# Kernel tuning notes

Measured on AMD Instinct MI355X. Metric: run time of the kernel, lower is better.

The kernel has to match this reference:

```python
import jax, jax.numpy as jnp
import numpy as np
import math

B, S, K, H, NH = 4, 1024, 512, 1024, 16
HD = H // NH  # 64


def _split_heads(x):
    # [B, L, H] -> [B, NH, L, HD]
    b, l, _ = x.shape
    return x.reshape(b, l, NH, HD).transpose(0, 2, 1, 3)


def setup_inputs() -> dict:
    key = jax.random.key(0)
    ks = jax.random.split(key, 16)
    scale = 1.0 / math.sqrt(H)
    d = {
        'hidden_states': jax.random.normal(ks[0], (B, S, H), jnp.float32),
        'encoder_hidden_states': jax.random.normal(ks[1], (B, K, H), jnp.float32),
        'attention_mask': jnp.zeros((B, 1, 1, S), jnp.float32),
        'encoder_attention_mask': jnp.zeros((B, 1, 1, K), jnp.float32),
    }
    names = ['q', 'k', 'v', 'kq', 'kk', 'kv']
    for i, n in enumerate(names):
        d[f'W{n}'] = jax.random.normal(ks[2 + i], (H, H), jnp.float32) * scale
        d[f'b{n}'] = jnp.zeros((H,), jnp.float32)
    return d


def reference(hidden_states, encoder_hidden_states, attention_mask, encoder_attention_mask,
              Wq, bq, Wk, bk, Wv, bv, Wkq, bkq, Wkk, bkk, Wkv, bkv):
    inv = 1.0 / math.sqrt(HD)
    # self branch
    q = _split_heads(hidden_states @ Wq + bq)            # [B,NH,S,HD]
    k = _split_heads(hidden_states @ Wk + bk)
    v = _split_heads(hidden_states @ Wv + bv)
    scores = jnp.einsum('bhsd,bhtd->bhst', q, k) * inv + attention_mask
    probs = jax.nn.softmax(scores, axis=-1)              # [B,NH,S,S]
    ctx = jnp.einsum('bhst,bhtd->bhsd', probs, v)
    # knowledge branch
    kq = _split_heads(hidden_states @ Wkq + bkq)          # [B,NH,S,HD]
    kk = _split_heads(encoder_hidden_states @ Wkk + bkk)  # [B,NH,K,HD]
    kv = _split_heads(encoder_hidden_states @ Wkv + bkv)
    kscores = jnp.einsum('bhsd,bhtd->bhst', kq, kk) * inv + encoder_attention_mask
    kprobs = jax.nn.softmax(kscores, axis=-1)            # [B,NH,S,K]
    kctx = jnp.einsum('bhst,bhtd->bhsd', kprobs, kv)
    # merge heads and average branches
    out = (ctx + kctx) * 0.5                             # [B,NH,S,HD]
    out = out.transpose(0, 2, 1, 3).reshape(B, S, H)
    return out
```

## Files before the change

kernel.cpp:

```cpp
#include <hip/hip_runtime.h>

#define BATCH 4
#define SEQ   1024
#define KENC  512
#define HDIM  1024
#define NHEAD 16
#define HD    64
#define LOG2E 1.44269504088896340736f

typedef __attribute__((ext_vector_type(8))) short bf16x8;
typedef __attribute__((ext_vector_type(4))) float f32x4;
typedef __attribute__((ext_vector_type(16))) float f32x16;
typedef __attribute__((ext_vector_type(4))) float f4v;
typedef __attribute__((ext_vector_type(4))) short s4v;

__device__ __forceinline__ short f2bf(float f) {
  unsigned u = __float_as_uint(f);
  u += 0x7fffu + ((u >> 16) & 1u);
  return (short)(u >> 16);
}

__device__ __forceinline__ void gload_lds16(const void* g, void* l) {
  __builtin_amdgcn_global_load_lds(
      (const __attribute__((address_space(1))) void*)g,
      (__attribute__((address_space(3))) void*)l, 16, 0, 0);
}

#define MF(A, B, C) __builtin_amdgcn_mfma_f32_16x16x32_bf16((A), (B), (C), 0, 0, 0)

__global__ __launch_bounds__(256) void cast2(const float* __restrict__ sa,
                                             short* __restrict__ da, int n4a,
                                             const float* __restrict__ sb,
                                             short* __restrict__ db, int n4b) {
  int i = blockIdx.x * 256 + threadIdx.x;
  const float* s;
  short* d;
  int j;
  if (i < n4a) { s = sa; d = da; j = i; }
  else { j = i - n4a; if (j >= n4b) return; s = sb; d = db; }
  f4v v = ((const f4v*)s)[j];
  s4v o;
#pragma unroll
  for (int k = 0; k < 4; ++k) o[k] = f2bf(v[k]);
  ((s4v*)d)[j] = o;
}

struct WtArgs { const float* W[6]; };

__global__ __launch_bounds__(256) void wt_cast(WtArgs a, short* __restrict__ wt) {
  int j = blockIdx.z;
  const float* W = a.W[j];
  short* dst = wt + (size_t)j * (HDIM * HDIM);
  int cb = blockIdx.x * 32, rb = blockIdx.y * 32;
  __shared__ float t[32][33];
  int tx = threadIdx.x & 31, ty = threadIdx.x >> 5;
#pragma unroll
  for (int rr = 0; rr < 4; ++rr)
    t[ty + rr * 8][tx] = W[(size_t)(rb + ty + rr * 8) * HDIM + cb + tx];
  __syncthreads();
#pragma unroll
  for (int rr = 0; rr < 4; ++rr)
    dst[(size_t)(cb + ty + rr * 8) * HDIM + rb + tx] = f2bf(t[tx][ty + rr * 8]);
}

struct ProjArgs {
  const short* X[6];
  const short* Wt[6];
  const float* bias[6];
  short* out[6];
  int tshift[6];
  int mode[6];
  float scale[6];
};

__global__ __launch_bounds__(256) void proj_gemm(ProjArgs a) {
  int lid = blockIdx.x;
  int t = (lid & 7) * 160 + (lid >> 3);
  int job, bx, by;
  if (t < 1024) { job = t >> 8; int r = t & 255; bx = r & 7; by = r >> 3; }
  else { int u = t - 1024; job = 4 + (u >> 7); int r = u & 127; bx = r & 7; by = r >> 3; }

  const short* X = a.X[job];
  const short* W = a.Wt[job];

  __shared__ __align__(16) char Lds[65536];

  int tid = threadIdx.x, lane = tid & 63, wave = tid >> 6;
  int wr = wave >> 1, wc = wave & 1;
  int l15 = lane & 15, g4 = lane >> 4;

  f32x4 acc[4][4];
#pragma unroll
  for (int m = 0; m < 4; ++m)
#pragma unroll
    for (int n = 0; n < 4; ++n)
#pragma unroll
      for (int r = 0; r < 4; ++r) acc[m][n][r] = 0.0f;

  int arow = by * 128, brow = bx * 128;
  const int crow = lane >> 2;
  const int sgrp = (lane & 3) ^ ((lane >> 2) & 3) ^ (lane >> 4);
  const int rsw = (lane & 3) ^ (l15 >> 2);

  const char* Xb = (const char*)X;
  const char* Wb = (const char*)W;
  const size_t sac0 = ((size_t)(arow + 32 * wave + crow) * HDIM + sgrp * 8) * 2;
  const size_t sac1 = sac0 + (size_t)16 * HDIM * 2;
  const size_t sbc0 = ((size_t)(brow + 32 * wave + crow) * HDIM + sgrp * 8) * 2;
  const size_t sbc1 = sbc0 + (size_t)16 * HDIM * 2;
  const int ldA0 = wave * 2048, ldA1 = ldA0 + 1024;
  const int ldB0 = 8192 + ldA0, ldB1 = ldB0 + 1024;

  const int aoff = wr * 4096 + l15 * 64 + ((g4 ^ rsw) << 4);
  const int boff = 8192 + wc * 4096 + l15 * 64 + ((g4 ^ rsw) << 4);

#define STG_A(SBO, SKT)                                                  \
  do {                                                                   \
    gload_lds16(Xb + sac0 + (size_t)(SKT) * 64, Lds + (SBO) + ldA0);     \
    gload_lds16(Xb + sac1 + (size_t)(SKT) * 64, Lds + (SBO) + ldA1);     \
  } while (0)
#define STG_B(SBO, SKT)                                                  \
  do {                                                                   \
    gload_lds16(Wb + sbc0 + (size_t)(SKT) * 64, Lds + (SBO) + ldB0);     \
    gload_lds16(Wb + sbc1 + (size_t)(SKT) * 64, Lds + (SBO) + ldB1);     \
  } while (0)

  STG_A(0, 0);     STG_B(0, 0);
  STG_A(16384, 1); STG_B(16384, 1);
  STG_A(32768, 2); STG_B(32768, 2);
  asm volatile("s_waitcnt vmcnt(8)" ::: "memory");
  __builtin_amdgcn_s_barrier();
  asm volatile("" ::: "memory");

#define STEP(BO, DO_STG, SBO, SKT, VMW, ENDBAR)                               \
  do {                                                                        \
                   \
    bf16x8 a0 = *(const bf16x8*)(Lds + (BO) + 0 * 1024 + aoff);               \
    bf16x8 a1 = *(const bf16x8*)(Lds + (BO) + 1 * 1024 + aoff);               \
    bf16x8 b0 = *(const bf16x8*)(Lds + (BO) + 0 * 1024 + boff);               \
    bf16x8 b1 = *(const bf16x8*)(Lds + (BO) + 1 * 1024 + boff);               \
    bf16x8 b2 = *(const bf16x8*)(Lds + (BO) + 2 * 1024 + boff);               \
    bf16x8 b3 = *(const bf16x8*)(Lds + (BO) + 3 * 1024 + boff);               \
    if (DO_STG) STG_A(SBO, SKT);                                              \
    __builtin_amdgcn_sched_barrier(0);                                        \
    __builtin_amdgcn_s_barrier();                                             \
    asm volatile("s_waitcnt lgkmcnt(0)" ::: "memory");                        \
    __builtin_amdgcn_sched_barrier(0);                                        \
    __builtin_amdgcn_s_setprio(1);                                            \
    acc[0][0] = MF(a0, b0, acc[0][0]);                                        \
    acc[0][1] = MF(a0, b1, acc[0][1]);                                        \
    acc[0][2] = MF(a0, b2, acc[0][2]);                                        \
    acc[0][3] = MF(a0, b3, acc[0][3]);                                        \
    acc[1][0] = MF(a1, b0, acc[1][0]);                                        \
    acc[1][1] = MF(a1, b1, acc[1][1]);                                        \
    acc[1][2] = MF(a1, b2, acc[1][2]);                                        \
    acc[1][3] = MF(a1, b3, acc[1][3]);                                        \
    __builtin_amdgcn_s_setprio(0);                                            \
    __builtin_amdgcn_sched_barrier(0);                                        \
    __builtin_amdgcn_s_barrier();                                             \
                    \
    bf16x8 a2 = *(const bf16x8*)(Lds + (BO) + 2 * 1024 + aoff);               \
    bf16x8 a3 = *(const bf16x8*)(Lds + (BO) + 3 * 1024 + aoff);               \
    if (DO_STG) STG_B(SBO, SKT);                                              \
    __builtin_amdgcn_sched_barrier(0);                                        \
    __builtin_amdgcn_s_barrier();                                             \
    asm volatile("s_waitcnt lgkmcnt(0)" ::: "memory");                        \
    __builtin_amdgcn_sched_barrier(0);                                        \
    __builtin_amdgcn_s_setprio(1);                                            \
    acc[2][0] = MF(a2, b0, acc[2][0]);                                        \
    acc[2][1] = MF(a2, b1, acc[2][1]);                                        \
    acc[2][2] = MF(a2, b2, acc[2][2]);                                        \
    acc[2][3] = MF(a2, b3, acc[2][3]);                                        \
    acc[3][0] = MF(a3, b0, acc[3][0]);                                        \
    acc[3][1] = MF(a3, b1, acc[3][1]);                                        \
    acc[3][2] = MF(a3, b2, acc[3][2]);                                        \
    acc[3][3] = MF(a3, b3, acc[3][3]);                                        \
    __builtin_amdgcn_s_setprio(0);                                            \
    asm volatile(VMW ::: "memory");                                           \
    __builtin_amdgcn_sched_barrier(0);                                        \
    if (ENDBAR) {                                                             \
      __builtin_amdgcn_s_barrier();                                           \
      asm volatile("" ::: "memory");                                          \
    }                                                                         \
  } while (0)

#pragma unroll 1
  for (int tt = 0; tt < 29; ++tt) {
    int bo = (tt & 3) << 14;
    int sbo = ((tt + 3) & 3) << 14;
    STEP(bo, 1, sbo, tt + 3, "s_waitcnt vmcnt(8)", 1);
  }
  STEP((29 & 3) << 14, 0, 0, 0, "s_waitcnt vmcnt(4)", 1);
  STEP((30 & 3) << 14, 0, 0, 0, "s_waitcnt vmcnt(0)", 1);
  STEP((31 & 3) << 14, 0, 0, 0, "s_nop 0", 0);

#undef STEP
#undef STG_A
#undef STG_B

  const float* bias = a.bias[job];
  short* out = a.out[job];
  int tshift = a.tshift[job], tmask = (1 << tshift) - 1, mode = a.mode[job];
  float scl = a.scale[job];
#pragma unroll
  for (int m = 0; m < 4; ++m) {
    int rowb = arow + wr * 64 + m * 16 + (g4 << 2);
#pragma unroll
    for (int n = 0; n < 4; ++n) {
      int col = brow + wc * 64 + n * 16 + l15;
      float bv = bias[col];
      int head = col >> 6, d = col & 63;
#pragma unroll
      for (int r = 0; r < 4; ++r) {
        int row = rowb + r;
        int bb = row >> tshift, tk = row & tmask;
        float val = (acc[m][n][r] + bv) * scl;
        size_t idx;
        if (mode == 0)
          idx = ((((size_t)bb * NHEAD + head) << tshift) + tk) * 64 + d;
        else
          idx = ((((size_t)bb * NHEAD + head) * 64 + d) << tshift) + tk;
        out[idx] = f2bf(val);
      }
    }
  }
}

__global__ __launch_bounds__(256, 3) void attn32(
    const short* __restrict__ qall, const short* __restrict__ kall,
    const short* __restrict__ vTall, const short* __restrict__ kqall,
    const short* __restrict__ kkall, const short* __restrict__ kvTall,
    const float* __restrict__ amask, const float* __restrict__ emask,
    float* __restrict__ out) {
  __shared__ char KT[2][8192];
  __shared__ char VT[2][8192];
  __shared__ float red[4][32];

  int lid = blockIdx.x;
  int id = (lid & 7) * 64 + (lid >> 3);
  int bh = id >> 3, qb = id & 7;
  int b = bh >> 4, h = bh & 15;
  int lane = threadIdx.x & 63, wave = threadIdx.x >> 6;
  int l31 = lane & 31, hi = lane >> 5, x7 = l31 & 7;
  int qrow0 = qb * 128 + wave * 32;

  bf16x8 qcur[4];
  {
    const short* qp = qall + ((size_t)bh * SEQ + qrow0 + l31) * 64;
#pragma unroll
    for (int i = 0; i < 4; ++i)
      qcur[i] = *(const bf16x8*)(qp + i * 16 + hi * 8);
  }

  const char* kb0 = (const char*)(kall + (size_t)bh * SEQ * 64);
  const char* vb0 = (const char*)(vTall + (size_t)bh * 64 * SEQ);
  const char* kb1 = (const char*)(kkall + (size_t)bh * KENC * 64);
  const char* vb1 = (const char*)(kvTall + (size_t)bh * 64 * KENC);
  const float* mpc = amask + (size_t)b * SEQ;

  auto STAGE = [&](int pb, const char* kb, const char* vb, size_t vrowb, int kt) {
    int t0 = threadIdx.x;
#pragma unroll
    for (int c = 0; c < 2; ++c) {
      int idx = c * 256 + t0;
      int row = idx >> 3, phys = idx & 7;
      int lg = phys ^ (row & 7);
      gload_lds16(kb + ((size_t)(kt * 64 + row)) * 128 + lg * 16,
                  KT[pb] + idx * 16);
      gload_lds16(vb + (size_t)row * vrowb + (size_t)kt * 128 + lg * 16,
                  VT[pb] + idx * 16);
    }
  };

  STAGE(0, kb0, vb0, SEQ * 2, 0);

  f32x16 ctx0, ctx1, c10, c11;
#pragma unroll
  for (int r = 0; r < 16; ++r) { ctx0[r] = 0.f; ctx1[r] = 0.f; c10[r] = 0.f; c11[r] = 0.f; }
  float mr = -1e30f, lr = 0.f;

#pragma unroll 1
  for (int t = 0; t < 24; ++t) {
    int p = t & 1;
    __syncthreads();
    if (t < 23) {
      int tn = t + 1;
      if (tn >= 16) STAGE(p ^ 1, kb1, vb1, KENC * 2, tn - 16);
      else          STAGE(p ^ 1, kb0, vb0, SEQ * 2, tn);
    }
    if (t == 16) {
      if (!hi) red[wave][l31] = lr;
      asm volatile("s_waitcnt lgkmcnt(0)" ::: "memory");
#pragma unroll
      for (int r2 = 0; r2 < 4; ++r2) {
        f4v lv = *(const f4v*)(&red[wave][r2 * 8 + 4 * hi]);
#pragma unroll
        for (int j2 = 0; j2 < 4; ++j2) {
          float li = __builtin_amdgcn_rcpf(lv[j2]);
          int r = r2 * 4 + j2;
          c10[r] = ctx0[r] * li;  ctx0[r] = 0.f;
          c11[r] = ctx1[r] * li;  ctx1[r] = 0.f;
        }
      }
      mr = -1e30f; lr = 0.f;
      const short* kqp = kqall + ((size_t)bh * SEQ + qrow0 + l31) * 64;
#pragma unroll
      for (int i = 0; i < 4; ++i)
        qcur[i] = *(const bf16x8*)(kqp + i * 16 + hi * 8);
      mpc = emask + (size_t)b * KENC;
    }
    int kt = (t >= 16) ? t - 16 : t;
    const char* Kp = KT[p];
    const char* Vp = VT[p];

    f32x16 s0, s1;
#pragma unroll
    for (int r = 0; r < 16; ++r) { s0[r] = 0.f; s1[r] = 0.f; }
    __builtin_amdgcn_s_setprio(1);
#pragma unroll
    for (int i = 0; i < 4; ++i) {
      bf16x8 kf = *(const bf16x8*)(Kp + (l31)*128 + (((2 * i + hi) ^ x7) << 4));
      s0 = __builtin_amdgcn_mfma_f32_32x32x16_bf16(kf, qcur[i], s0, 0, 0, 0);
    }
#pragma unroll
    for (int i = 0; i < 4; ++i) {
      bf16x8 kf = *(const bf16x8*)(Kp + (32 + l31) * 128 + (((2 * i + hi) ^ x7) << 4));
      s1 = __builtin_amdgcn_mfma_f32_32x32x16_bf16(kf, qcur[i], s1, 0, 0, 0);
    }
    __builtin_amdgcn_s_setprio(0);

    const float* mp = mpc + kt * 64;
#pragma unroll
    for (int r2 = 0; r2 < 4; ++r2) {
      f4v ma = *(const f4v*)(mp + r2 * 8 + 4 * hi);
      f4v mb = *(const f4v*)(mp + 32 + r2 * 8 + 4 * hi);
#pragma unroll
      for (int j2 = 0; j2 < 4; ++j2) {
        s0[r2 * 4 + j2] = fmaf(ma[j2], LOG2E, s0[r2 * 4 + j2]);
        s1[r2 * 4 + j2] = fmaf(mb[j2], LOG2E, s1[r2 * 4 + j2]);
      }
    }

    float mx = s0[0];
#pragma unroll
    for (int r = 1; r < 16; ++r) mx = fmaxf(mx, s0[r]);
#pragma unroll
    for (int r = 0; r < 16; ++r) mx = fmaxf(mx, s1[r]);
    mx = fmaxf(mx, __int_as_float(__shfl_xor(__float_as_int(mx), 32)));

    if (!__all(mx <= mr + 12.f)) {
      float mn = fmaxf(mr, mx);
      float scl = __builtin_amdgcn_exp2f(mr - mn);
      mr = mn; lr *= scl;
      if (!hi) red[wave][l31] = scl;
      asm volatile("s_waitcnt lgkmcnt(0)" ::: "memory");
#pragma unroll
      for (int r2 = 0; r2 < 4; ++r2) {
        f4v sv = *(const f4v*)(&red[wave][r2 * 8 + 4 * hi]);
#pragma unroll
        for (int j2 = 0; j2 < 4; ++j2) {
          ctx0[r2 * 4 + j2] *= sv[j2];
          ctx1[r2 * 4 + j2] *= sv[j2];
        }
      }
    }

    float rs = 0.f;
#pragma unroll
    for (int r = 0; r < 16; ++r) { s0[r] = __builtin_amdgcn_exp2f(s0[r] - mr); rs += s0[r]; }
#pragma unroll
    for (int r = 0; r < 16; ++r) { s1[r] = __builtin_amdgcn_exp2f(s1[r] - mr); rs += s1[r]; }
    rs += __int_as_float(__shfl_xor(__float_as_int(rs), 32));
    lr += rs;

#pragma unroll
    for (int s = 0; s < 2; ++s) {
      const f32x16& sv = s ? s1 : s0;
      unsigned W[8];
#pragma unroll
      for (int r2 = 0; r2 < 4; ++r2) {
        asm("v_cvt_pk_bf16_f32 %0, %1, %2"
            : "=v"(W[r2 * 2]) : "v"(sv[r2 * 4 + 0]), "v"(sv[r2 * 4 + 1]));
        asm("v_cvt_pk_bf16_f32 %0, %1, %2"
            : "=v"(W[r2 * 2 + 1]) : "v"(sv[r2 * 4 + 2]), "v"(sv[r2 * 4 + 3]));
      }
#pragma unroll
      for (int jr = 0; jr < 2; ++jr) {
        unsigned sendA = hi ? W[(2 * jr) * 2]     : W[(2 * jr + 1) * 2];
        unsigned sendB = hi ? W[(2 * jr) * 2 + 1] : W[(2 * jr + 1) * 2 + 1];
        unsigned rA = (unsigned)__shfl_xor((int)sendA, 32);
        unsigned rB = (unsigned)__shfl_xor((int)sendB, 32);
        union { unsigned u[4]; bf16x8 v; } pa;
        if (!hi) { pa.u[0] = W[2 * jr * 2]; pa.u[1] = W[2 * jr * 2 + 1];
                   pa.u[2] = rA;            pa.u[3] = rB; }
        else     { pa.u[0] = rA;            pa.u[1] = rB;
                   pa.u[2] = W[(2 * jr + 1) * 2]; pa.u[3] = W[(2 * jr + 1) * 2 + 1]; }
        int j = s * 2 + jr;
        __builtin_amdgcn_s_setprio(1);
        bf16x8 vf0 = *(const bf16x8*)(Vp + (l31)*128 + (((2 * j + hi) ^ x7) << 4));
        ctx0 = __builtin_amdgcn_mfma_f32_32x32x16_bf16(pa.v, vf0, ctx0, 0, 0, 0);
        bf16x8 vf1 = *(const bf16x8*)(Vp + (32 + l31) * 128 + (((2 * j + hi) ^ x7) << 4));
        ctx1 = __builtin_amdgcn_mfma_f32_32x32x16_bf16(pa.v, vf1, ctx1, 0, 0, 0);
        __builtin_amdgcn_s_setprio(0);
      }
    }
  }

  if (!hi) red[wave][l31] = lr;
  asm volatile("s_waitcnt lgkmcnt(0)" ::: "memory");
  float* op = out + ((size_t)b * SEQ) * HDIM + h * 64 + l31;
#pragma unroll
  for (int r2 = 0; r2 < 4; ++r2) {
    f4v lv = *(const f4v*)(&red[wave][r2 * 8 + 4 * hi]);
#pragma unroll
    for (int j2 = 0; j2 < 4; ++j2) {
      float li = __builtin_amdgcn_rcpf(lv[j2]);
      int s = qrow0 + r2 * 8 + 4 * hi + j2;
      int r = r2 * 4 + j2;
      op[(size_t)s * HDIM]      = 0.5f * (c10[r] + ctx0[r] * li);
      op[(size_t)s * HDIM + 32] = 0.5f * (c11[r] + ctx1[r] * li);
    }
  }
}

extern "C" void kernel_launch(void* const* d_in, const int* in_sizes, int n_in,
                              void* d_out, int out_size, void* d_ws, size_t ws_size,
                              hipStream_t stream) {
  const float* hid = (const float*)d_in[0];
  const float* enc = (const float*)d_in[1];
  const float* amask = (const float*)d_in[2];
  const float* emask = (const float*)d_in[3];

  char* ws = (char*)d_ws;
  short* hbf = (short*)(ws);
  short* ebf = (short*)(ws + (8u << 20));
  short* wt = (short*)(ws + (12u << 20));
  short* qo = (short*)(ws + (24u << 20));
  short* ko = (short*)(ws + (32u << 20));
  short* vT = (short*)(ws + (40u << 20));
  short* kqo = (short*)(ws + (48u << 20));
  short* kko = (short*)(ws + (56u << 20));
  short* kvT = (short*)(ws + (60u << 20));

  cast2<<<6144, 256, 0, stream>>>(hid, hbf, (BATCH * SEQ * HDIM) / 4,
                                  enc, ebf, (BATCH * KENC * HDIM) / 4);

  WtArgs wa;
  for (int j = 0; j < 6; ++j) wa.W[j] = (const float*)d_in[4 + 2 * j];
  wt_cast<<<dim3(32, 32, 6), 256, 0, stream>>>(wa, wt);

  ProjArgs pa;
  const short* Xs[6] = {hbf, hbf, hbf, hbf, ebf, ebf};
  short* outs[6] = {qo, ko, vT, kqo, kko, kvT};
  const int tsh[6] = {10, 10, 10, 10, 9, 9};
  const int md[6] = {0, 0, 1, 0, 0, 1};
  const float qscale = 0.125f * LOG2E;
  const float scl[6] = {qscale, 1.f, 1.f, qscale, 1.f, 1.f};
  for (int j = 0; j < 6; ++j) {
    pa.X[j] = Xs[j];
    pa.Wt[j] = wt + (size_t)j * (HDIM * HDIM);
    pa.bias[j] = (const float*)d_in[5 + 2 * j];
    pa.out[j] = outs[j];
    pa.tshift[j] = tsh[j];
    pa.mode[j] = md[j];
    pa.scale[j] = scl[j];
  }
  proj_gemm<<<1280, 256, 0, stream>>>(pa);

  attn32<<<512, 256, 0, stream>>>(qo, ko, vT, kqo, kko, kvT, amask, emask,
                                  (float*)d_out);
}
```

Before: 151.1 us.

## Simplify GEMM main-loop barriers and load V fragments directly from global memory

In the projection GEMM, all A and B fragments are now read from LDS up front, and A and B are staged together. This removes the mid-step barriers and lgkmcnt waits that split each K-step into two halves. In the attention kernel, the V tile is no longer staged through LDS. Each lane instead loads its V fragments straight from global memory into registers at the top of every tile iteration, and launch bounds drop from 3 to 2 blocks per CU. This cuts LDS traffic and synchronization, at the cost of more registers, exposed global-load latency, and possibly less occupancy.

```diff
diff --git a/kernel.cpp b/kernel.cpp
--- a/kernel.cpp
+++ b/kernel.cpp
@@ -114,38 +114,32 @@
   const int aoff = wr * 4096 + l15 * 64 + ((g4 ^ rsw) << 4);
   const int boff = 8192 + wc * 4096 + l15 * 64 + ((g4 ^ rsw) << 4);
 
-#define STG_A(SBO, SKT)                                                  \
+#define STG_AB(SBO, SKT)                                                 \
   do {                                                                   \
     gload_lds16(Xb + sac0 + (size_t)(SKT) * 64, Lds + (SBO) + ldA0);     \
     gload_lds16(Xb + sac1 + (size_t)(SKT) * 64, Lds + (SBO) + ldA1);     \
-  } while (0)
-#define STG_B(SBO, SKT)                                                  \
-  do {                                                                   \
     gload_lds16(Wb + sbc0 + (size_t)(SKT) * 64, Lds + (SBO) + ldB0);     \
     gload_lds16(Wb + sbc1 + (size_t)(SKT) * 64, Lds + (SBO) + ldB1);     \
   } while (0)
 
-  STG_A(0, 0);     STG_B(0, 0);
-  STG_A(16384, 1); STG_B(16384, 1);
-  STG_A(32768, 2); STG_B(32768, 2);
+  STG_AB(0, 0);
+  STG_AB(16384, 1);
+  STG_AB(32768, 2);
   asm volatile("s_waitcnt vmcnt(8)" ::: "memory");
   __builtin_amdgcn_s_barrier();
   asm volatile("" ::: "memory");
 
 #define STEP(BO, DO_STG, SBO, SKT, VMW, ENDBAR)                               \
   do {                                                                        \
-                   \
     bf16x8 a0 = *(const bf16x8*)(Lds + (BO) + 0 * 1024 + aoff);               \
     bf16x8 a1 = *(const bf16x8*)(Lds + (BO) + 1 * 1024 + aoff);               \
+    bf16x8 a2 = *(const bf16x8*)(Lds + (BO) + 2 * 1024 + aoff);               \
+    bf16x8 a3 = *(const bf16x8*)(Lds + (BO) + 3 * 1024 + aoff);               \
     bf16x8 b0 = *(const bf16x8*)(Lds + (BO) + 0 * 1024 + boff);               \
     bf16x8 b1 = *(const bf16x8*)(Lds + (BO) + 1 * 1024 + boff);               \
     bf16x8 b2 = *(const bf16x8*)(Lds + (BO) + 2 * 1024 + boff);               \
     bf16x8 b3 = *(const bf16x8*)(Lds + (BO) + 3 * 1024 + boff);               \
-    if (DO_STG) STG_A(SBO, SKT);                                              \
-    __builtin_amdgcn_sched_barrier(0);                                        \
-    __builtin_amdgcn_s_barrier();                                             \
-    asm volatile("s_waitcnt lgkmcnt(0)" ::: "memory");                        \
-    __builtin_amdgcn_sched_barrier(0);                                        \
+    if (DO_STG) STG_AB(SBO, SKT);                                             \
     __builtin_amdgcn_s_setprio(1);                                            \
     acc[0][0] = MF(a0, b0, acc[0][0]);                                        \
     acc[0][1] = MF(a0, b1, acc[0][1]);                                        \
@@ -155,18 +149,6 @@
     acc[1][1] = MF(a1, b1, acc[1][1]);                                        \
     acc[1][2] = MF(a1, b2, acc[1][2]);                                        \
     acc[1][3] = MF(a1, b3, acc[1][3]);                                        \
-    __builtin_amdgcn_s_setprio(0);                                            \
-    __builtin_amdgcn_sched_barrier(0);                                        \
-    __builtin_amdgcn_s_barrier();                                             \
-                    \
-    bf16x8 a2 = *(const bf16x8*)(Lds + (BO) + 2 * 1024 + aoff);               \
-    bf16x8 a3 = *(const bf16x8*)(Lds + (BO) + 3 * 1024 + aoff);               \
-    if (DO_STG) STG_B(SBO, SKT);                                              \
-    __builtin_amdgcn_sched_barrier(0);                                        \
-    __builtin_amdgcn_s_barrier();                                             \
-    asm volatile("s_waitcnt lgkmcnt(0)" ::: "memory");                        \
-    __builtin_amdgcn_sched_barrier(0);                                        \
-    __builtin_amdgcn_s_setprio(1);                                            \
     acc[2][0] = MF(a2, b0, acc[2][0]);                                        \
     acc[2][1] = MF(a2, b1, acc[2][1]);                                        \
     acc[2][2] = MF(a2, b2, acc[2][2]);                                        \
@@ -177,7 +159,6 @@
     acc[3][3] = MF(a3, b3, acc[3][3]);                                        \
     __builtin_amdgcn_s_setprio(0);                                            \
     asm volatile(VMW ::: "memory");                                           \
-    __builtin_amdgcn_sched_barrier(0);                                        \
     if (ENDBAR) {                                                             \
       __builtin_amdgcn_s_barrier();                                           \
       asm volatile("" ::: "memory");                                          \
@@ -195,8 +176,7 @@
   STEP((31 & 3) << 14, 0, 0, 0, "s_nop 0", 0);
 
 #undef STEP
-#undef STG_A
-#undef STG_B
+#undef STG_AB
 
   const float* bias = a.bias[job];
   short* out = a.out[job];
@@ -226,14 +206,13 @@
   }
 }
 
-__global__ __launch_bounds__(256, 3) void attn32(
+__global__ __launch_bounds__(256, 2) void attn32(
     const short* __restrict__ qall, const short* __restrict__ kall,
     const short* __restrict__ vTall, const short* __restrict__ kqall,
     const short* __restrict__ kkall, const short* __restrict__ kvTall,
     const float* __restrict__ amask, const float* __restrict__ emask,
     float* __restrict__ out) {
   __shared__ char KT[2][8192];
-  __shared__ char VT[2][8192];
   __shared__ float red[4][32];
 
   int lid = blockIdx.x;
@@ -258,7 +237,7 @@
   const char* vb1 = (const char*)(kvTall + (size_t)bh * 64 * KENC);
   const float* mpc = amask + (size_t)b * SEQ;
 
-  auto STAGE = [&](int pb, const char* kb, const char* vb, size_t vrowb, int kt) {
+  auto STAGE_K = [&](int pb, const char* kb, int kt) {
     int t0 = threadIdx.x;
 #pragma unroll
     for (int c = 0; c < 2; ++c) {
@@ -267,12 +246,10 @@
       int lg = phys ^ (row & 7);
       gload_lds16(kb + ((size_t)(kt * 64 + row)) * 128 + lg * 16,
                   KT[pb] + idx * 16);
-      gload_lds16(vb + (size_t)row * vrowb + (size_t)kt * 128 + lg * 16,
-                  VT[pb] + idx * 16);
     }
   };
 
-  STAGE(0, kb0, vb0, SEQ * 2, 0);
+  STAGE_K(0, kb0, 0);
 
   f32x16 ctx0, ctx1, c10, c11;
 #pragma unroll
@@ -283,10 +260,28 @@
   for (int t = 0; t < 24; ++t) {
     int p = t & 1;
     __syncthreads();
+
+    int kt = (t >= 16) ? t - 16 : t;
+    const char* vbc = (t >= 16) ? vb1 : vb0;
+    size_t vstride = (size_t)((t >= 16) ? KENC : SEQ) * 2;
+    bf16x8 v00, v01, v02, v03, v10, v11, v12, v13;
+    {
+      const char* vrow0 = vbc + (size_t)l31 * vstride + (size_t)kt * 128 + hi * 16;
+      const char* vrow1 = vrow0 + 32 * vstride;
+      v00 = *(const bf16x8*)(vrow0);
+      v01 = *(const bf16x8*)(vrow0 + 32);
+      v02 = *(const bf16x8*)(vrow0 + 64);
+      v03 = *(const bf16x8*)(vrow0 + 96);
+      v10 = *(const bf16x8*)(vrow1);
+      v11 = *(const bf16x8*)(vrow1 + 32);
+      v12 = *(const bf16x8*)(vrow1 + 64);
+      v13 = *(const bf16x8*)(vrow1 + 96);
+    }
+
     if (t < 23) {
       int tn = t + 1;
-      if (tn >= 16) STAGE(p ^ 1, kb1, vb1, KENC * 2, tn - 16);
-      else          STAGE(p ^ 1, kb0, vb0, SEQ * 2, tn);
+      if (tn >= 16) STAGE_K(p ^ 1, kb1, tn - 16);
+      else          STAGE_K(p ^ 1, kb0, tn);
     }
     if (t == 16) {
       if (!hi) red[wave][l31] = lr;
@@ -309,9 +304,7 @@
         qcur[i] = *(const bf16x8*)(kqp + i * 16 + hi * 8);
       mpc = emask + (size_t)b * KENC;
     }
-    int kt = (t >= 16) ? t - 16 : t;
     const char* Kp = KT[p];
-    const char* Vp = VT[p];
 
     f32x16 s0, s1;
 #pragma unroll
@@ -396,10 +389,10 @@
         else     { pa.u[0] = rA;            pa.u[1] = rB;
                    pa.u[2] = W[(2 * jr + 1) * 2]; pa.u[3] = W[(2 * jr + 1) * 2 + 1]; }
         int j = s * 2 + jr;
+        bf16x8 vf0 = (j == 0) ? v00 : (j == 1) ? v01 : (j == 2) ? v02 : v03;
+        bf16x8 vf1 = (j == 0) ? v10 : (j == 1) ? v11 : (j == 2) ? v12 : v13;
         __builtin_amdgcn_s_setprio(1);
-        bf16x8 vf0 = *(const bf16x8*)(Vp + (l31)*128 + (((2 * j + hi) ^ x7) << 4));
         ctx0 = __builtin_amdgcn_mfma_f32_32x32x16_bf16(pa.v, vf0, ctx0, 0, 0, 0);
-        bf16x8 vf1 = *(const bf16x8*)(Vp + (32 + l31) * 128 + (((2 * j + hi) ^ x7) << 4));
         ctx1 = __builtin_amdgcn_mfma_f32_32x32x16_bf16(pa.v, vf1, ctx1, 0, 0, 0);
         __builtin_amdgcn_s_setprio(0);
       }
```

Result: slower. 180.5 us (+19.5%).

## Merge cast kernels, simplify GEMM grid and collapse pipeline stages

Applied to the files above, without the earlier changes.

Fuses the weight-transpose cast and the activation cast into one prep kernel, which saves a launch. The projection GEMM now uses a plain 3D grid (8,32,6) and returns early for the out-of-range row blocks of the encoder jobs, replacing the XCD-aware swizzled block mapping. Inside the K loop, the two half-steps with their intermediate barriers and lgkmcnt waits are collapsed into one phase that loads all A/B fragments up front and issues all four global-to-LDS loads together. This cuts barriers, but it loses the block-to-XCD locality mapping and launches idle blocks. It may also leave an LDS buffer reuse hazard, since the loads are issued before the current fragments are known to be consumed by every wave.

```diff
diff --git a/kernel.cpp b/kernel.cpp
--- a/kernel.cpp
+++ b/kernel.cpp
@@ -28,39 +28,42 @@
 
 #define MF(A, B, C) __builtin_amdgcn_mfma_f32_16x16x32_bf16((A), (B), (C), 0, 0, 0)
 
-__global__ __launch_bounds__(256) void cast2(const float* __restrict__ sa,
-                                             short* __restrict__ da, int n4a,
-                                             const float* __restrict__ sb,
-                                             short* __restrict__ db, int n4b) {
-  int i = blockIdx.x * 256 + threadIdx.x;
-  const float* s;
-  short* d;
-  int j;
-  if (i < n4a) { s = sa; d = da; j = i; }
-  else { j = i - n4a; if (j >= n4b) return; s = sb; d = db; }
-  f4v v = ((const f4v*)s)[j];
-  s4v o;
-#pragma unroll
-  for (int k = 0; k < 4; ++k) o[k] = f2bf(v[k]);
-  ((s4v*)d)[j] = o;
-}
-
-struct WtArgs { const float* W[6]; };
-
-__global__ __launch_bounds__(256) void wt_cast(WtArgs a, short* __restrict__ wt) {
-  int j = blockIdx.z;
-  const float* W = a.W[j];
-  short* dst = wt + (size_t)j * (HDIM * HDIM);
-  int cb = blockIdx.x * 32, rb = blockIdx.y * 32;
+struct PrepArgs { const float* W[6]; };
+
+__global__ __launch_bounds__(256) void prep(PrepArgs a, short* __restrict__ wt,
+                                            const float* __restrict__ hid,
+                                            short* __restrict__ hbf, int n4h,
+                                            const float* __restrict__ enc,
+                                            short* __restrict__ ebf, int n4e) {
   __shared__ float t[32][33];
-  int tx = threadIdx.x & 31, ty = threadIdx.x >> 5;
-#pragma unroll
-  for (int rr = 0; rr < 4; ++rr)
-    t[ty + rr * 8][tx] = W[(size_t)(rb + ty + rr * 8) * HDIM + cb + tx];
-  __syncthreads();
-#pragma unroll
-  for (int rr = 0; rr < 4; ++rr)
-    dst[(size_t)(cb + ty + rr * 8) * HDIM + rb + tx] = f2bf(t[tx][ty + rr * 8]);
+  int blk = blockIdx.x;
+  if (blk < 6144) {
+    int j = blk >> 10;
+    int r = blk & 1023;
+    int cb = (r & 31) * 32, rb = (r >> 5) * 32;
+    const float* W = a.W[j];
+    short* dst = wt + (size_t)j * (HDIM * HDIM);
+    int tx = threadIdx.x & 31, ty = threadIdx.x >> 5;
+#pragma unroll
+    for (int rr = 0; rr < 4; ++rr)
+      t[ty + rr * 8][tx] = W[(size_t)(rb + ty + rr * 8) * HDIM + cb + tx];
+    __syncthreads();
+#pragma unroll
+    for (int rr = 0; rr < 4; ++rr)
+      dst[(size_t)(cb + ty + rr * 8) * HDIM + rb + tx] = f2bf(t[tx][ty + rr * 8]);
+  } else {
+    int i = (blk - 6144) * 256 + threadIdx.x;
+    const float* s;
+    short* d;
+    int j;
+    if (i < n4h) { s = hid; d = hbf; j = i; }
+    else { j = i - n4h; if (j >= n4e) return; s = enc; d = ebf; }
+    f4v v = ((const f4v*)s)[j];
+    s4v o;
+#pragma unroll
+    for (int k = 0; k < 4; ++k) o[k] = f2bf(v[k]);
+    ((s4v*)d)[j] = o;
+  }
 }
 
 struct ProjArgs {
@@ -68,18 +71,18 @@
   const short* Wt[6];
   const float* bias[6];
   short* out[6];
+  int M[6];
   int tshift[6];
   int mode[6];
   float scale[6];
 };
 
 __global__ __launch_bounds__(256) void proj_gemm(ProjArgs a) {
-  int lid = blockIdx.x;
-  int t = (lid & 7) * 160 + (lid >> 3);
-  int job, bx, by;
-  if (t < 1024) { job = t >> 8; int r = t & 255; bx = r & 7; by = r >> 3; }
-  else { int u = t - 1024; job = 4 + (u >> 7); int r = u & 127; bx = r & 7; by = r >> 3; }
-
+  int job = blockIdx.z;
+  int M = a.M[job];
+  int by = blockIdx.y;
+  if (by * 128 >= M) return;
+  int bx = blockIdx.x;
   const short* X = a.X[job];
   const short* W = a.Wt[job];
 
@@ -114,38 +117,32 @@
   const int aoff = wr * 4096 + l15 * 64 + ((g4 ^ rsw) << 4);
   const int boff = 8192 + wc * 4096 + l15 * 64 + ((g4 ^ rsw) << 4);
 
-#define STG_A(SBO, SKT)                                                  \
+#define STG_AB(SBO, SKT)                                                 \
   do {                                                                   \
     gload_lds16(Xb + sac0 + (size_t)(SKT) * 64, Lds + (SBO) + ldA0);     \
     gload_lds16(Xb + sac1 + (size_t)(SKT) * 64, Lds + (SBO) + ldA1);     \
-  } while (0)
-#define STG_B(SBO, SKT)                                                  \
-  do {                                                                   \
     gload_lds16(Wb + sbc0 + (size_t)(SKT) * 64, Lds + (SBO) + ldB0);     \
     gload_lds16(Wb + sbc1 + (size_t)(SKT) * 64, Lds + (SBO) + ldB1);     \
   } while (0)
 
-  STG_A(0, 0);     STG_B(0, 0);
-  STG_A(16384, 1); STG_B(16384, 1);
-  STG_A(32768, 2); STG_B(32768, 2);
+  STG_AB(0, 0);
+  STG_AB(16384, 1);
+  STG_AB(32768, 2);
   asm volatile("s_waitcnt vmcnt(8)" ::: "memory");
   __builtin_amdgcn_s_barrier();
   asm volatile("" ::: "memory");
 
 #define STEP(BO, DO_STG, SBO, SKT, VMW, ENDBAR)                               \
   do {                                                                        \
-                   \
     bf16x8 a0 = *(const bf16x8*)(Lds + (BO) + 0 * 1024 + aoff);               \
     bf16x8 a1 = *(const bf16x8*)(Lds + (BO) + 1 * 1024 + aoff);               \
+    bf16x8 a2 = *(const bf16x8*)(Lds + (BO) + 2 * 1024 + aoff);               \
+    bf16x8 a3 = *(const bf16x8*)(Lds + (BO) + 3 * 1024 + aoff);               \
     bf16x8 b0 = *(const bf16x8*)(Lds + (BO) + 0 * 1024 + boff);               \
     bf16x8 b1 = *(const bf16x8*)(Lds + (BO) + 1 * 1024 + boff);               \
     bf16x8 b2 = *(const bf16x8*)(Lds + (BO) + 2 * 1024 + boff);               \
     bf16x8 b3 = *(const bf16x8*)(Lds + (BO) + 3 * 1024 + boff);               \
-    if (DO_STG) STG_A(SBO, SKT);                                              \
-    __builtin_amdgcn_sched_barrier(0);                                        \
-    __builtin_amdgcn_s_barrier();                                             \
-    asm volatile("s_waitcnt lgkmcnt(0)" ::: "memory");                        \
-    __builtin_amdgcn_sched_barrier(0);                                        \
+    if (DO_STG) STG_AB(SBO, SKT);                                             \
     __builtin_amdgcn_s_setprio(1);                                            \
     acc[0][0] = MF(a0, b0, acc[0][0]);                                        \
     acc[0][1] = MF(a0, b1, acc[0][1]);                                        \
@@ -155,18 +152,6 @@
     acc[1][1] = MF(a1, b1, acc[1][1]);                                        \
     acc[1][2] = MF(a1, b2, acc[1][2]);                                        \
     acc[1][3] = MF(a1, b3, acc[1][3]);                                        \
-    __builtin_amdgcn_s_setprio(0);                                            \
-    __builtin_amdgcn_sched_barrier(0);                                        \
-    __builtin_amdgcn_s_barrier();                                             \
-                    \
-    bf16x8 a2 = *(const bf16x8*)(Lds + (BO) + 2 * 1024 + aoff);               \
-    bf16x8 a3 = *(const bf16x8*)(Lds + (BO) + 3 * 1024 + aoff);               \
-    if (DO_STG) STG_B(SBO, SKT);                                              \
-    __builtin_amdgcn_sched_barrier(0);                                        \
-    __builtin_amdgcn_s_barrier();                                             \
-    asm volatile("s_waitcnt lgkmcnt(0)" ::: "memory");                        \
-    __builtin_amdgcn_sched_barrier(0);                                        \
-    __builtin_amdgcn_s_setprio(1);                                            \
     acc[2][0] = MF(a2, b0, acc[2][0]);                                        \
     acc[2][1] = MF(a2, b1, acc[2][1]);                                        \
     acc[2][2] = MF(a2, b2, acc[2][2]);                                        \
@@ -177,7 +162,6 @@
     acc[3][3] = MF(a3, b3, acc[3][3]);                                        \
     __builtin_amdgcn_s_setprio(0);                                            \
     asm volatile(VMW ::: "memory");                                           \
-    __builtin_amdgcn_sched_barrier(0);                                        \
     if (ENDBAR) {                                                             \
       __builtin_amdgcn_s_barrier();                                           \
       asm volatile("" ::: "memory");                                          \
@@ -195,8 +179,7 @@
   STEP((31 & 3) << 14, 0, 0, 0, "s_nop 0", 0);
 
 #undef STEP
-#undef STG_A
-#undef STG_B
+#undef STG_AB
 
   const float* bias = a.bias[job];
   short* out = a.out[job];
@@ -442,16 +425,15 @@
   short* kko = (short*)(ws + (56u << 20));
   short* kvT = (short*)(ws + (60u << 20));
 
-  cast2<<<6144, 256, 0, stream>>>(hid, hbf, (BATCH * SEQ * HDIM) / 4,
+  PrepArgs wa;
+  for (int j = 0; j < 6; ++j) wa.W[j] = (const float*)d_in[4 + 2 * j];
+  prep<<<12288, 256, 0, stream>>>(wa, wt, hid, hbf, (BATCH * SEQ * HDIM) / 4,
                                   enc, ebf, (BATCH * KENC * HDIM) / 4);
-
-  WtArgs wa;
-  for (int j = 0; j < 6; ++j) wa.W[j] = (const float*)d_in[4 + 2 * j];
-  wt_cast<<<dim3(32, 32, 6), 256, 0, stream>>>(wa, wt);
 
   ProjArgs pa;
   const short* Xs[6] = {hbf, hbf, hbf, hbf, ebf, ebf};
   short* outs[6] = {qo, ko, vT, kqo, kko, kvT};
+  const int Ms[6] = {4096, 4096, 4096, 4096, 2048, 2048};
   const int tsh[6] = {10, 10, 10, 10, 9, 9};
   const int md[6] = {0, 0, 1, 0, 0, 1};
   const float qscale = 0.125f * LOG2E;
@@ -461,11 +443,12 @@
     pa.Wt[j] = wt + (size_t)j * (HDIM * HDIM);
     pa.bias[j] = (const float*)d_in[5 + 2 * j];
     pa.out[j] = outs[j];
+    pa.M[j] = Ms[j];
     pa.tshift[j] = tsh[j];
     pa.mode[j] = md[j];
     pa.scale[j] = scl[j];
   }
-  proj_gemm<<<1280, 256, 0, stream>>>(pa);
+  proj_gemm<<<dim3(8, 32, 6), 256, 0, stream>>>(pa);
 
   attn32<<<512, 256, 0, stream>>>(qo, ko, vT, kqo, kko, kvT, amask, emask,
                                   (float*)d_out);
```

Measured after the change: 152.9 us. Within noise of the previous version (+1.2%).
